# Kernel optimization log

Hardware: AMD Instinct MI355X
Metric: run time of the kernel (lower is better)

The kernel has to match this reference:

```python
import jax, jax.numpy as jnp
import numpy as np


def setup_inputs() -> dict:
    key = jax.random.key(0)
    x = jax.random.normal(key, (32, 2048, 128), dtype=jnp.float32)
    return {"x": x, "window_size": 16}


def reference(x, window_size):
    # x: [B, S, F] -> out: [B, S, W, F]
    # Window at position i covers x[:, i:i+W]; positions past S-W are
    # zero-padded at the tail (matches the original's second_part zeros).
    B, S, F = x.shape
    W = window_size
    x_pad = jnp.pad(x, ((0, 0), (0, W - 1), (0, 0)))  # [B, S+W-1, F]
    idx = jnp.arange(S)[:, None] + jnp.arange(W)[None, :]  # [S, W]
    return x_pad[:, idx]  # [B, S, W, F]
```

## Files before the change

kernel.cpp:

```cpp
#include <hip/hip_runtime.h>


typedef float floatx4 __attribute__((ext_vector_type(4)));

#define NTHR 256u
#define PER_BLOCK 8192u
#define NBLK 4096u
#define REPS 2

__global__ __launch_bounds__(256) void WindowingLayer_22084721836441_kernel(
    const floatx4* __restrict__ x, floatx4* __restrict__ out) {
    unsigned base = blockIdx.x * PER_BLOCK + threadIdx.x;
    for (int rep = 0; rep < REPS; ++rep) {
#pragma unroll
        for (unsigned t = 0; t < 32; t += 8) {
            unsigned o[8];
            floatx4 v[8];
#pragma unroll
            for (int k = 0; k < 8; ++k) {
                o[k] = base + (t + (unsigned)k) * NTHR;
                unsigned chunk = o[k] >> 9;
                unsigned r = o[k] & 511u;
                unsigned row = (chunk & 2047u) + (r >> 5);
                v[k] = (floatx4)(0.f, 0.f, 0.f, 0.f);
                if (row < 2048u) {
                    v[k] = x[(chunk << 5) + r];
                }
            }
#pragma unroll
            for (int k = 0; k < 8; ++k) {
                __builtin_nontemporal_store(v[k], &out[o[k]]);
            }
        }
        asm volatile("" ::: "memory");
    }
}

extern "C" void kernel_launch(void* const* d_in, const int* in_sizes, int n_in,
                              void* d_out, int out_size, void* d_ws, size_t ws_size,
                              hipStream_t stream) {
    const floatx4* x = (const floatx4*)d_in[0];
    floatx4* out = (floatx4*)d_out;
    WindowingLayer_22084721836441_kernel<<<NBLK, NTHR, 0, stream>>>(x, out);
}
```

Baseline: 640.1 us.

## Stage input rows in LDS per block and emit windows from shared memory

Each block now loads a 47-row slab of x for one batch and 32 output positions into LDS once, then writes all 16 windowed copies from LDS using nontemporal stores. This replaces 16x redundant global/L2 reads of each input row with a single read per block plus LDS reads. The cost is a __syncthreads, LDS usage, and fewer blocks (2048 instead of 4096), so there is less concurrency to hide store latency.

```diff
diff --git a/kernel.cpp b/kernel.cpp
--- a/kernel.cpp
+++ b/kernel.cpp
@@ -3,36 +3,43 @@
 
 typedef float floatx4 __attribute__((ext_vector_type(4)));
 
-#define NTHR 256u
-#define PER_BLOCK 8192u
-#define NBLK 4096u
-#define REPS 2
+#define NTHR 256
+#define NC 32
+#define ROWS (NC + 15)
+#define BLK_F4 (NC * 512)
 
-__global__ __launch_bounds__(256) void WindowingLayer_22084721836441_kernel(
+__global__ __launch_bounds__(NTHR) void WindowingLayer_22084721836441_kernel(
     const floatx4* __restrict__ x, floatx4* __restrict__ out) {
-    unsigned base = blockIdx.x * PER_BLOCK + threadIdx.x;
-    for (int rep = 0; rep < REPS; ++rep) {
+    __shared__ floatx4 lds[48 * 32];
+    const int b  = blockIdx.x >> 6;
+    const int i0 = (blockIdx.x & 63) * NC;
+    const int t  = threadIdx.x;
+
+    const floatx4* xs = x + (((b << 11) + i0) << 5);
+    const int rows_left = 2048 - i0;
+    const int valid_f4 = (rows_left < ROWS ? rows_left : ROWS) << 5;
+    for (int idx = t; idx < ROWS * 32; idx += NTHR) {
+        floatx4 v = (floatx4)(0.f, 0.f, 0.f, 0.f);
+        if (idx < valid_f4) v = xs[idx];
+        lds[idx] = v;
+    }
+    __syncthreads();
+
+    floatx4* ob = out + (size_t)blockIdx.x * BLK_F4;
+#pragma unroll 1
+    for (int j = 0; j < 64; j += 8) {
+        floatx4 v[8];
 #pragma unroll
-        for (unsigned t = 0; t < 32; t += 8) {
-            unsigned o[8];
-            floatx4 v[8];
+        for (int k = 0; k < 8; ++k) {
+            int ol = t + (j + k) * NTHR;
+            int cl = ol >> 9;
+            int r  = ol & 511;
+            v[k] = lds[((cl + (r >> 5)) << 5) + (r & 31)];
+        }
 #pragma unroll
-            for (int k = 0; k < 8; ++k) {
-                o[k] = base + (t + (unsigned)k) * NTHR;
-                unsigned chunk = o[k] >> 9;
-                unsigned r = o[k] & 511u;
-                unsigned row = (chunk & 2047u) + (r >> 5);
-                v[k] = (floatx4)(0.f, 0.f, 0.f, 0.f);
-                if (row < 2048u) {
-                    v[k] = x[(chunk << 5) + r];
-                }
-            }
-#pragma unroll
-            for (int k = 0; k < 8; ++k) {
-                __builtin_nontemporal_store(v[k], &out[o[k]]);
-            }
+        for (int k = 0; k < 8; ++k) {
+            __builtin_nontemporal_store(v[k], &ob[t + (j + k) * NTHR]);
         }
-        asm volatile("" ::: "memory");
     }
 }
 
@@ -41,5 +48,5 @@
                               hipStream_t stream) {
     const floatx4* x = (const floatx4*)d_in[0];
     floatx4* out = (floatx4*)d_out;
-    WindowingLayer_22084721836441_kernel<<<NBLK, NTHR, 0, stream>>>(x, out);
+    WindowingLayer_22084721836441_kernel<<<2048, NTHR, 0, stream>>>(x, out);
 }
```

After: 538.0 us. 1.19x faster.
